# Kernel tuning notes

Hardware: AMD Instinct MI355X
Metric: run time of the kernel (lower is better)

Reference implementation:

```python
import jax, jax.numpy as jnp
import numpy as np

M, N, DIM = 128, 128, 256
BS = 8192
START_SIGMA = max(M, N) / 2.0
EPOCHS = 20.0
START_LR = 0.5
TAU = EPOCHS / np.log(START_SIGMA)


def setup_inputs() -> dict:
    key = jax.random.key(0)
    k_data, k_w = jax.random.split(key)
    data = jax.random.normal(k_data, (BS, DIM), dtype=jnp.float32)
    all_weights = jax.random.normal(k_w, (M, N, DIM), dtype=jnp.float32)
    return {"data": data, "all_weights": all_weights, "it": 3}


def reference(data, all_weights, it):
    m, n, dim = all_weights.shape
    bs = data.shape[0]

    # decayed sigma and learning rate (scalar schedule)
    sigma = START_SIGMA * jnp.exp(-jnp.float32(it) / jnp.float32(TAU))
    lr = START_LR * jnp.exp(-jnp.float32(it) / jnp.float32(EPOCHS))

    # pairwise Euclidean distances: [bs, m*n]
    w_flat = all_weights.reshape(m * n, dim)
    x_sq = jnp.sum(data * data, axis=1, keepdims=True)            # [bs, 1]
    w_sq = jnp.sum(w_flat * w_flat, axis=1)[None, :]              # [1, m*n]
    dists = jnp.sqrt(x_sq + w_sq - 2.0 * data @ w_flat.T)         # [bs, m*n]

    # best-matching unit grid coordinates (unravel over (m, n))
    bmu = jnp.argmin(dists, axis=1)                               # [bs]
    wins0 = (bmu // n).astype(jnp.float32)                        # row coord
    wins1 = (bmu % n).astype(jnp.float32)                         # col coord

    # Gaussian neighborhood around BMU, scaled by lr: [bs, m, n]
    d = 2.0 * sigma * sigma
    rows = jnp.arange(m, dtype=jnp.float32)
    cols = jnp.arange(n, dtype=jnp.float32)
    px = jnp.exp(-(rows[None, :] - wins0[:, None]) ** 2 / d)      # [bs, m]
    py = jnp.exp(-(cols[None, :] - wins1[:, None]) ** 2 / d)      # [bs, n]
    neighbor = (px[:, :, None] * py[:, None, :]) * lr             # [bs, m, n]

    # weighted batch update of the codebook
    denom = jnp.sum(neighbor, axis=0)[..., None]                  # [m, n, 1]
    numer = jnp.einsum('bk,bd->kd', neighbor.reshape(bs, m * n), data)
    numer = numer.reshape(m, n, dim)                              # [m, n, dim]
    new_weights = jnp.where(denom != 0, numer / denom, all_weights)
    return new_weights
```

## Files before the change

kernel.cpp:

```cpp
#include <hip/hip_runtime.h>
#include <hip/hip_fp16.h>

#define BS    8192
#define DIM   256
#define KTOT  16384
#define SLOTS 256
#define MARGIN 1.0f

typedef __attribute__((ext_vector_type(8))) _Float16 half8;
typedef __attribute__((ext_vector_type(4))) float f32x4;
typedef unsigned long long u64;

__device__ inline ushort f2h(float f) { return __half_as_ushort(__float2half(f)); }

__device__ inline void gload_lds16(const void* g, void* l) {
    __builtin_amdgcn_global_load_lds(
        (const __attribute__((address_space(1))) unsigned int*)g,
        (__attribute__((address_space(3))) unsigned int*)l, 16, 0, 0);
}

__device__ inline unsigned int fmap(float f) {
    unsigned int b = __float_as_uint(f);
    return (b & 0x80000000u) ? ~b : (b | 0x80000000u);
}
__device__ inline float unfmap(unsigned int m) {
    return (m & 0x80000000u) ? __uint_as_float(m & 0x7FFFFFFFu)
                             : __uint_as_float(~m);
}

__global__ void setup_all_kernel(float* __restrict__ S, float* __restrict__ G,
                                 float* __restrict__ cntf, unsigned int* __restrict__ keys,
                                 u64* __restrict__ keys2, unsigned int* __restrict__ cslot,
                                 const int* __restrict__ itp) {
    int idx = blockIdx.x * 256 + threadIdx.x;
    *(float4*)&S[(size_t)idx * 4] = make_float4(0.f, 0.f, 0.f, 0.f);
    if (idx < KTOT) {
        float itf = (float)itp[0];
        const float START_SIGMA = 64.0f;
        const float TAU = (float)(20.0 / 4.1588830833596715);
        float sigma = START_SIGMA * expf(-itf / TAU);
        float d2 = 2.0f * sigma * sigma;
        int i = idx >> 7, j = idx & 127;
        float diff = (float)(i - j);
        G[idx] = expf(-(diff * diff) / d2);
        cntf[idx] = 0.f;
    }
    if (idx < BS) { keys[idx] = 0xFFFFFFFFu; keys2[idx] = ~0ULL; cslot[idx] = 0u; }
}

__global__ void cvt_all_kernel(const float* __restrict__ x, const float* __restrict__ w,
                               ushort* __restrict__ xf, ushort* __restrict__ wf,
                               float* __restrict__ wsq) {
    int wid = threadIdx.x >> 6, lane = threadIdx.x & 63;
    int row = blockIdx.x * 4 + wid;
    int h = lane * 4;
    int window = h >> 5, c = (h >> 3) & 3, off = h & 7;
    if (row < BS) {
        int swpos = (window << 5) + (((c ^ ((row >> 1) & 3)) << 3)) + off;
        float4 v = *(const float4*)&x[(size_t)row * DIM + h];
        ushort4 hv;
        hv.x = f2h(v.x); hv.y = f2h(v.y); hv.z = f2h(v.z); hv.w = f2h(v.w);
        *(ushort4*)&xf[(size_t)row * DIM + swpos] = hv;
    } else {
        int r = row - BS;
        int swpos = (window << 5) + (((c ^ ((r >> 1) & 3)) << 3)) + off;
        float4 v = *(const float4*)&w[(size_t)r * DIM + h];
        ushort4 hv;
        hv.x = f2h(v.x); hv.y = f2h(v.y); hv.z = f2h(v.z); hv.w = f2h(v.w);
        *(ushort4*)&wf[(size_t)r * DIM + swpos] = hv;
        float s = v.x * v.x + v.y * v.y + v.z * v.z + v.w * v.w;
        #pragma unroll
        for (int o = 32; o; o >>= 1) s += __shfl_down(s, o, 64);
        if (lane == 0) wsq[r] = s;
    }
}

__global__ __launch_bounds__(256) void bmu_seed_kernel(
    const ushort* __restrict__ xf, const ushort* __restrict__ wf,
    const float* __restrict__ wsq, unsigned int* __restrict__ keys) {
    __shared__ ushort A[128 * 32];
    __shared__ ushort B[128 * 32];
    __shared__ float red[128][2];

    int m0 = blockIdx.x * 128;
    int k0 = blockIdx.y * 1024;
    int tid = threadIdx.x, w = tid >> 6, lane = tid & 63;
    int wm = (w & 1) * 64, wn = (w >> 1) * 64;
    int lm = lane & 15, quad = lane >> 4;
    int sw = (quad ^ ((lm >> 1) & 3)) * 8;
    int srow = lane >> 2, scol = (lane & 3) * 8;

    f32x4 acc[4][4];
    #pragma unroll
    for (int mi = 0; mi < 4; ++mi)
        #pragma unroll
        for (int ni = 0; ni < 4; ++ni)
            acc[mi][ni] = (f32x4){0.f, 0.f, 0.f, 0.f};

    for (int kb = 0; kb < DIM; kb += 32) {
        size_t axoff = (size_t)(m0 + w * 32 + srow) * DIM + kb + scol;
        size_t bxoff = (size_t)(k0 + w * 32 + srow) * DIM + kb + scol;
        gload_lds16(xf + axoff,            &A[(w * 32) * 32]);
        gload_lds16(xf + axoff + 16 * DIM, &A[(w * 32 + 16) * 32]);
        gload_lds16(wf + bxoff,            &B[(w * 32) * 32]);
        gload_lds16(wf + bxoff + 16 * DIM, &B[(w * 32 + 16) * 32]);
        __syncthreads();
        half8 av[4], bv[4];
        #pragma unroll
        for (int mi = 0; mi < 4; ++mi)
            av[mi] = *(const half8*)&A[(wm + mi * 16 + lm) * 32 + sw];
        #pragma unroll
        for (int ni = 0; ni < 4; ++ni)
            bv[ni] = *(const half8*)&B[(wn + ni * 16 + lm) * 32 + sw];
        #pragma unroll
        for (int mi = 0; mi < 4; ++mi)
            #pragma unroll
            for (int ni = 0; ni < 4; ++ni)
                acc[mi][ni] = __builtin_amdgcn_mfma_f32_16x16x32_f16(
                    av[mi], bv[ni], acc[mi][ni], 0, 0, 0);
        __syncthreads();
    }
    float wsqv[4];
    #pragma unroll
    for (int ni = 0; ni < 4; ++ni) wsqv[ni] = wsq[k0 + wn + ni * 16 + lm];
    #pragma unroll
    for (int mi = 0; mi < 4; ++mi)
        #pragma unroll
        for (int r = 0; r < 4; ++r) {
            float b = 3.4e38f;
            #pragma unroll
            for (int ni = 0; ni < 4; ++ni)
                b = fminf(b, fmaf(-2.0f, acc[mi][ni][r], wsqv[ni]));
            #pragma unroll
            for (int mask = 1; mask < 16; mask <<= 1)
                b = fminf(b, __shfl_xor(b, mask, 64));
            if (lm == 0) red[wm + mi * 16 + quad * 4 + r][w >> 1] = b;
        }
    __syncthreads();
    if (tid < 128)
        atomicMin(&keys[m0 + tid], fmap(fminf(red[tid][0], red[tid][1])));
}

__global__ __launch_bounds__(256) void bmu_fused_kernel(
    const ushort* __restrict__ xf, const ushort* __restrict__ wf,
    const float* __restrict__ wsq, const unsigned int* __restrict__ keys,
    unsigned int* __restrict__ cand, unsigned int* __restrict__ cslot) {
    __shared__ ushort A[128 * 32];
    __shared__ ushort B[128 * 32];
    __shared__ float thr_l[16][256];

    int m0 = blockIdx.x * 128;
    int kbase = blockIdx.y * 1024;
    int tid = threadIdx.x, w = tid >> 6, lane = tid & 63;
    int wm = (w & 1) * 64, wn = (w >> 1) * 64;
    int lm = lane & 15, quad = lane >> 4;
    int sw = (quad ^ ((lm >> 1) & 3)) * 8;
    int srow = lane >> 2, scol = (lane & 3) * 8;

    #pragma unroll
    for (int mi = 0; mi < 4; ++mi)
        #pragma unroll
        for (int r = 0; r < 4; ++r)
            thr_l[mi * 4 + r][tid] =
                unfmap(keys[m0 + wm + mi * 16 + quad * 4 + r]) + MARGIN;

    for (int kt = 0; kt < 8; ++kt) {
        int k0 = kbase + kt * 128;
        f32x4 acc[4][4];
        #pragma unroll
        for (int mi = 0; mi < 4; ++mi)
            #pragma unroll
            for (int ni = 0; ni < 4; ++ni)
                acc[mi][ni] = (f32x4){0.f, 0.f, 0.f, 0.f};

        for (int kb = 0; kb < DIM; kb += 32) {
            size_t axoff = (size_t)(m0 + w * 32 + srow) * DIM + kb + scol;
            size_t bxoff = (size_t)(k0 + w * 32 + srow) * DIM + kb + scol;
            gload_lds16(xf + axoff,            &A[(w * 32) * 32]);
            gload_lds16(xf + axoff + 16 * DIM, &A[(w * 32 + 16) * 32]);
            gload_lds16(wf + bxoff,            &B[(w * 32) * 32]);
            gload_lds16(wf + bxoff + 16 * DIM, &B[(w * 32 + 16) * 32]);
            __syncthreads();
            half8 av[4], bv[4];
            #pragma unroll
            for (int mi = 0; mi < 4; ++mi)
                av[mi] = *(const half8*)&A[(wm + mi * 16 + lm) * 32 + sw];
            #pragma unroll
            for (int ni = 0; ni < 4; ++ni)
                bv[ni] = *(const half8*)&B[(wn + ni * 16 + lm) * 32 + sw];
            #pragma unroll
            for (int mi = 0; mi < 4; ++mi)
                #pragma unroll
                for (int ni = 0; ni < 4; ++ni)
                    acc[mi][ni] = __builtin_amdgcn_mfma_f32_16x16x32_f16(
                        av[mi], bv[ni], acc[mi][ni], 0, 0, 0);
            __syncthreads();
        }
        float wsqv[4];
        #pragma unroll
        for (int ni = 0; ni < 4; ++ni) wsqv[ni] = wsq[k0 + wn + ni * 16 + lm];
        #pragma unroll
        for (int mi = 0; mi < 4; ++mi)
            #pragma unroll
            for (int r = 0; r < 4; ++r) {
                float thr = thr_l[mi * 4 + r][tid];
                #pragma unroll
                for (int ni = 0; ni < 4; ++ni) {
                    float sc = fmaf(-2.0f, acc[mi][ni][r], wsqv[ni]);
                    if (sc <= thr) {
                        unsigned int s =
                            (unsigned int)(m0 + wm + mi * 16 + quad * 4 + r);
                        unsigned int idx = atomicAdd(&cslot[s], 1u);
                        if (idx < SLOTS)
                            cand[(size_t)s * SLOTS + idx] =
                                (unsigned int)(k0 + wn + ni * 16 + lm);
                    }
                }
            }
    }
}

__global__ __launch_bounds__(256) void bmu_refine_kernel(
    const float* __restrict__ x, const float* __restrict__ w,
    const unsigned int* __restrict__ cand, const unsigned int* __restrict__ cslot,
    u64* __restrict__ keys2) {
    int lane = threadIdx.x & 63;
    int s = blockIdx.x * 4 + (threadIdx.x >> 6);
    unsigned int n = cslot[s];
    if (n > SLOTS) n = SLOTS;
    float4 xv = *(const float4*)&x[(size_t)s * DIM + lane * 4];
    u64 best = ~0ULL;
    for (unsigned int c = 0; c < n; ++c) {
        unsigned int k = cand[(size_t)s * SLOTS + c];
        float4 wv = *(const float4*)&w[(size_t)k * DIM + lane * 4];
        float dx = xv.x - wv.x, dy = xv.y - wv.y;
        float dz = xv.z - wv.z, dw = xv.w - wv.w;
        float d = dx * dx + dy * dy + dz * dz + dw * dw;
        #pragma unroll
        for (int off = 32; off; off >>= 1) d += __shfl_xor(d, off, 64);
        u64 key = ((u64)fmap(d) << 32) | (u64)k;
        best = (key < best) ? key : best;
    }
    if (lane == 0 && n > 0) keys2[s] = best;
}

__global__ __launch_bounds__(256) void scatter_kernel(
    const float* __restrict__ x, const u64* __restrict__ keys2,
    float* __restrict__ S, float* __restrict__ cntf) {
    int lane = threadIdx.x & 63;
    int s = blockIdx.x * 4 + (threadIdx.x >> 6);
    unsigned int k = (unsigned int)keys2[s];
    if (k >= KTOT) return;
    float4 xv = *(const float4*)&x[(size_t)s * DIM + lane * 4];
    float* Sp = &S[(size_t)k * DIM + lane * 4];
    atomicAdd(Sp + 0, xv.x);
    atomicAdd(Sp + 1, xv.y);
    atomicAdd(Sp + 2, xv.z);
    atomicAdd(Sp + 3, xv.w);
    if (lane == 0) atomicAdd(&cntf[k], 1.0f);
}

__global__ __launch_bounds__(256) void gemm1_kernel(
    const float* __restrict__ G, const float* __restrict__ S, float* __restrict__ T) {
    __shared__ float Sl[128 * 68];
    int n0 = blockIdx.x * 64;
    int tid = threadIdx.x;
    #pragma unroll
    for (int q = 0; q < 8; ++q) {
        int idx = q * 256 + tid;
        int row = idx >> 4, c4 = (idx & 15) * 4;
        *(float4*)&Sl[row * 68 + c4] = *(const float4*)&S[(size_t)row * 32768 + n0 + c4];
    }
    __syncthreads();
    int ng = tid & 15, ig = tid >> 4;
    for (int pass = 0; pass < 2; ++pass) {
        int ibase = pass * 64 + ig * 4;
        float acc[4][4] = {};
        for (int a = 0; a < 128; ++a) {
            float4 sv = *(const float4*)&Sl[a * 68 + ng * 4];
            #pragma unroll
            for (int ii = 0; ii < 4; ++ii) {
                float g = G[(ibase + ii) * 128 + a];
                acc[ii][0] = fmaf(g, sv.x, acc[ii][0]);
                acc[ii][1] = fmaf(g, sv.y, acc[ii][1]);
                acc[ii][2] = fmaf(g, sv.z, acc[ii][2]);
                acc[ii][3] = fmaf(g, sv.w, acc[ii][3]);
            }
        }
        #pragma unroll
        for (int ii = 0; ii < 4; ++ii)
            *(float4*)&T[(size_t)(ibase + ii) * 32768 + n0 + ng * 4] =
                *(float4*)&acc[ii][0];
    }
}

__global__ void denom_s1_kernel(const float* __restrict__ cntf, const float* __restrict__ G,
                                float* __restrict__ M1) {
    int a = blockIdx.x, j = threadIdx.x;
    float acc = 0.f;
    for (int b2 = 0; b2 < 128; ++b2)
        acc = fmaf(cntf[a * 128 + b2], G[b2 * 128 + j], acc);
    M1[a * 128 + j] = acc;
}

__global__ void denom_s2_kernel(const float* __restrict__ G, const float* __restrict__ M1,
                                float* __restrict__ denom) {
    int i = blockIdx.x, j = threadIdx.x;
    float acc = 0.f;
    for (int a = 0; a < 128; ++a)
        acc = fmaf(G[i * 128 + a], M1[a * 128 + j], acc);
    denom[i * 128 + j] = acc;
}

__global__ __launch_bounds__(256) void gemm2_fin_kernel(
    const float* __restrict__ G, const float* __restrict__ T,
    const float* __restrict__ denom, const float* __restrict__ w,
    float* __restrict__ out) {
    __shared__ float Tl[128 * 68];
    int i = blockIdx.x, dq = blockIdx.y;
    int tid = threadIdx.x;
    #pragma unroll
    for (int q = 0; q < 8; ++q) {
        int idx = q * 256 + tid;
        int row = idx >> 4, c4 = (idx & 15) * 4;
        *(float4*)&Tl[row * 68 + c4] =
            *(const float4*)&T[(size_t)i * 32768 + row * 256 + dq * 64 + c4];
    }
    __syncthreads();
    int dg = tid & 15, jg = tid >> 4;
    for (int pass = 0; pass < 2; ++pass) {
        int jbase = pass * 64 + jg * 4;
        float acc[4][4] = {};
        for (int b2 = 0; b2 < 128; ++b2) {
            float4 tv = *(const float4*)&Tl[b2 * 68 + dg * 4];
            #pragma unroll
            for (int jj = 0; jj < 4; ++jj) {
                float g = G[(jbase + jj) * 128 + b2];
                acc[jj][0] = fmaf(g, tv.x, acc[jj][0]);
                acc[jj][1] = fmaf(g, tv.y, acc[jj][1]);
                acc[jj][2] = fmaf(g, tv.z, acc[jj][2]);
                acc[jj][3] = fmaf(g, tv.w, acc[jj][3]);
            }
        }
        #pragma unroll
        for (int jj = 0; jj < 4; ++jj) {
            int j = jbase + jj;
            float dv = denom[i * 128 + j];
            size_t e = (size_t)(i * 128 + j) * DIM + dq * 64 + dg * 4;
            float4 r;
            if (dv != 0.0f) {
                float inv = 1.0f / dv;
                r.x = acc[jj][0] * inv; r.y = acc[jj][1] * inv;
                r.z = acc[jj][2] * inv; r.w = acc[jj][3] * inv;
            } else {
                r = *(const float4*)&w[e];
            }
            *(float4*)&out[e] = r;
        }
    }
}

extern "C" void kernel_launch(void* const* d_in, const int* in_sizes, int n_in,
                              void* d_out, int out_size, void* d_ws, size_t ws_size,
                              hipStream_t stream) {
    const float* data = (const float*)d_in[0];
    const float* w    = (const float*)d_in[1];
    const int*   itp  = (const int*)d_in[2];
    float* out = (float*)d_out;

    char* ws = (char*)d_ws;
    size_t off = 0;
    float*        wsq   = (float*)(ws + off);        off += 65536;
    unsigned int* keys  = (unsigned int*)(ws + off); off += 65536;
    u64*          keys2 = (u64*)(ws + off);          off += 65536;
    unsigned int* cslot = (unsigned int*)(ws + off); off += 65536;
    float*        G     = (float*)(ws + off);        off += 65536;
    float*        cntf  = (float*)(ws + off);        off += 65536;
    float*        M1    = (float*)(ws + off);        off += 65536;
    float*        denom = (float*)(ws + off);        off += 65536;
    ushort*       xf    = (ushort*)(ws + off);       off += 4194304;
    ushort*       wf    = (ushort*)(ws + off);       off += 8388608;
    u64*          spare = (u64*)(ws + off);          off += 1048576;
    float*        S     = (float*)(ws + off);        off += 16777216;
    float*        T     = (float*)(ws + off);        off += 16777216;
    unsigned int* cand  = (unsigned int*)T;
    (void)spare;

    setup_all_kernel<<<4096, 256, 0, stream>>>(S, G, cntf, keys, keys2, cslot, itp);
    cvt_all_kernel<<<(BS + KTOT) / 4, 256, 0, stream>>>(data, w, xf, wf, wsq);
    bmu_seed_kernel<<<dim3(64, 16), 256, 0, stream>>>(xf, wf, wsq, keys);
    bmu_fused_kernel<<<dim3(64, 16), 256, 0, stream>>>(xf, wf, wsq, keys, cand, cslot);
    bmu_refine_kernel<<<BS / 4, 256, 0, stream>>>(data, w, cand, cslot, keys2);
    scatter_kernel<<<BS / 4, 256, 0, stream>>>(data, keys2, S, cntf);
    gemm1_kernel<<<512, 256, 0, stream>>>(G, S, T);
    denom_s1_kernel<<<128, 128, 0, stream>>>(cntf, G, M1);
    denom_s2_kernel<<<128, 128, 0, stream>>>(G, M1, denom);
    gemm2_fin_kernel<<<dim3(128, 4), 256, 0, stream>>>(G, T, denom, w, out);
}
```

Measured before the change: 360.5 us.

## Fuse setup/convert, refine/scatter, and denominator into neighboring kernels

Merges the setup and fp16-convert kernels into one prep kernel, folds BMU refinement and scatter into a single kernel that drops the keys2 buffer, and computes the neighborhood denominator inside the final GEMM kernel instead of two separate launches. The bmu_fused threshold table shrinks from a per-thread 16x256 layout to 128 shared floats. The aim is to cut launch count and intermediate global traffic. In exchange, each of the 512 final-GEMM blocks recomputes two 128x128 mat-vec passes serially, and prep's S zeroing is now bounded by idx.

```diff
diff --git a/kernel.cpp b/kernel.cpp
--- a/kernel.cpp
+++ b/kernel.cpp
@@ -28,12 +28,15 @@
                              : __uint_as_float(~m);
 }
 
-__global__ void setup_all_kernel(float* __restrict__ S, float* __restrict__ G,
-                                 float* __restrict__ cntf, unsigned int* __restrict__ keys,
-                                 u64* __restrict__ keys2, unsigned int* __restrict__ cslot,
-                                 const int* __restrict__ itp) {
+__global__ void prep_kernel(const float* __restrict__ x, const float* __restrict__ w,
+                            ushort* __restrict__ xf, ushort* __restrict__ wf,
+                            float* __restrict__ wsq, float* __restrict__ S,
+                            float* __restrict__ G, float* __restrict__ cntf,
+                            unsigned int* __restrict__ keys, unsigned int* __restrict__ cslot,
+                            const int* __restrict__ itp) {
     int idx = blockIdx.x * 256 + threadIdx.x;
-    *(float4*)&S[(size_t)idx * 4] = make_float4(0.f, 0.f, 0.f, 0.f);
+    if (idx < 1048576)
+        *(float4*)&S[(size_t)idx * 4] = make_float4(0.f, 0.f, 0.f, 0.f);
     if (idx < KTOT) {
         float itf = (float)itp[0];
         const float START_SIGMA = 64.0f;
@@ -45,12 +48,8 @@
         G[idx] = expf(-(diff * diff) / d2);
         cntf[idx] = 0.f;
     }
-    if (idx < BS) { keys[idx] = 0xFFFFFFFFu; keys2[idx] = ~0ULL; cslot[idx] = 0u; }
-}
-
-__global__ void cvt_all_kernel(const float* __restrict__ x, const float* __restrict__ w,
-                               ushort* __restrict__ xf, ushort* __restrict__ wf,
-                               float* __restrict__ wsq) {
+    if (idx < BS) { keys[idx] = 0xFFFFFFFFu; cslot[idx] = 0u; }
+
     int wid = threadIdx.x >> 6, lane = threadIdx.x & 63;
     int row = blockIdx.x * 4 + wid;
     int h = lane * 4;
@@ -147,7 +146,7 @@
     unsigned int* __restrict__ cand, unsigned int* __restrict__ cslot) {
     __shared__ ushort A[128 * 32];
     __shared__ ushort B[128 * 32];
-    __shared__ float thr_l[16][256];
+    __shared__ float thr_l[128];
 
     int m0 = blockIdx.x * 128;
     int kbase = blockIdx.y * 1024;
@@ -157,12 +156,8 @@
     int sw = (quad ^ ((lm >> 1) & 3)) * 8;
     int srow = lane >> 2, scol = (lane & 3) * 8;
 
-    #pragma unroll
-    for (int mi = 0; mi < 4; ++mi)
-        #pragma unroll
-        for (int r = 0; r < 4; ++r)
-            thr_l[mi * 4 + r][tid] =
-                unfmap(keys[m0 + wm + mi * 16 + quad * 4 + r]) + MARGIN;
+    if (tid < 128) thr_l[tid] = unfmap(keys[m0 + tid]) + MARGIN;
+    __syncthreads();
 
     for (int kt = 0; kt < 8; ++kt) {
         int k0 = kbase + kt * 128;
@@ -203,13 +198,13 @@
         for (int mi = 0; mi < 4; ++mi)
             #pragma unroll
             for (int r = 0; r < 4; ++r) {
-                float thr = thr_l[mi * 4 + r][tid];
+                int rowi = wm + mi * 16 + quad * 4 + r;
+                float thr = thr_l[rowi];
                 #pragma unroll
                 for (int ni = 0; ni < 4; ++ni) {
                     float sc = fmaf(-2.0f, acc[mi][ni][r], wsqv[ni]);
                     if (sc <= thr) {
-                        unsigned int s =
-                            (unsigned int)(m0 + wm + mi * 16 + quad * 4 + r);
+                        unsigned int s = (unsigned int)(m0 + rowi);
                         unsigned int idx = atomicAdd(&cslot[s], 1u);
                         if (idx < SLOTS)
                             cand[(size_t)s * SLOTS + idx] =
@@ -220,10 +215,10 @@
     }
 }
 
-__global__ __launch_bounds__(256) void bmu_refine_kernel(
+__global__ __launch_bounds__(256) void refine_scatter_kernel(
     const float* __restrict__ x, const float* __restrict__ w,
     const unsigned int* __restrict__ cand, const unsigned int* __restrict__ cslot,
-    u64* __restrict__ keys2) {
+    float* __restrict__ S, float* __restrict__ cntf) {
     int lane = threadIdx.x & 63;
     int s = blockIdx.x * 4 + (threadIdx.x >> 6);
     unsigned int n = cslot[s];
@@ -241,17 +236,7 @@
         u64 key = ((u64)fmap(d) << 32) | (u64)k;
         best = (key < best) ? key : best;
     }
-    if (lane == 0 && n > 0) keys2[s] = best;
-}
-
-__global__ __launch_bounds__(256) void scatter_kernel(
-    const float* __restrict__ x, const u64* __restrict__ keys2,
-    float* __restrict__ S, float* __restrict__ cntf) {
-    int lane = threadIdx.x & 63;
-    int s = blockIdx.x * 4 + (threadIdx.x >> 6);
-    unsigned int k = (unsigned int)keys2[s];
-    if (k >= KTOT) return;
-    float4 xv = *(const float4*)&x[(size_t)s * DIM + lane * 4];
+    unsigned int k = (unsigned int)best;
     float* Sp = &S[(size_t)k * DIM + lane * 4];
     atomicAdd(Sp + 0, xv.x);
     atomicAdd(Sp + 1, xv.y);
@@ -294,37 +279,34 @@
     }
 }
 
-__global__ void denom_s1_kernel(const float* __restrict__ cntf, const float* __restrict__ G,
-                                float* __restrict__ M1) {
-    int a = blockIdx.x, j = threadIdx.x;
-    float acc = 0.f;
-    for (int b2 = 0; b2 < 128; ++b2)
-        acc = fmaf(cntf[a * 128 + b2], G[b2 * 128 + j], acc);
-    M1[a * 128 + j] = acc;
-}
-
-__global__ void denom_s2_kernel(const float* __restrict__ G, const float* __restrict__ M1,
-                                float* __restrict__ denom) {
-    int i = blockIdx.x, j = threadIdx.x;
-    float acc = 0.f;
-    for (int a = 0; a < 128; ++a)
-        acc = fmaf(G[i * 128 + a], M1[a * 128 + j], acc);
-    denom[i * 128 + j] = acc;
-}
-
 __global__ __launch_bounds__(256) void gemm2_fin_kernel(
     const float* __restrict__ G, const float* __restrict__ T,
-    const float* __restrict__ denom, const float* __restrict__ w,
+    const float* __restrict__ cntf, const float* __restrict__ w,
     float* __restrict__ out) {
     __shared__ float Tl[128 * 68];
+    __shared__ float Pl[128];
+    __shared__ float dl[128];
     int i = blockIdx.x, dq = blockIdx.y;
     int tid = threadIdx.x;
+    if (tid < 128) {
+        float p = 0.f;
+        for (int a = 0; a < 128; ++a)
+            p = fmaf(G[i * 128 + a], cntf[a * 128 + tid], p);
+        Pl[tid] = p;
+    }
     #pragma unroll
     for (int q = 0; q < 8; ++q) {
         int idx = q * 256 + tid;
         int row = idx >> 4, c4 = (idx & 15) * 4;
         *(float4*)&Tl[row * 68 + c4] =
             *(const float4*)&T[(size_t)i * 32768 + row * 256 + dq * 64 + c4];
+    }
+    __syncthreads();
+    if (tid < 128) {
+        float accd = 0.f;
+        for (int b2 = 0; b2 < 128; ++b2)
+            accd = fmaf(Pl[b2], G[b2 * 128 + tid], accd);
+        dl[tid] = accd;
     }
     __syncthreads();
     int dg = tid & 15, jg = tid >> 4;
@@ -345,7 +327,7 @@
         #pragma unroll
         for (int jj = 0; jj < 4; ++jj) {
             int j = jbase + jj;
-            float dv = denom[i * 128 + j];
+            float dv = dl[j];
             size_t e = (size_t)(i * 128 + j) * DIM + dq * 64 + dg * 4;
             float4 r;
             if (dv != 0.0f) {
@@ -372,28 +354,20 @@
     size_t off = 0;
     float*        wsq   = (float*)(ws + off);        off += 65536;
     unsigned int* keys  = (unsigned int*)(ws + off); off += 65536;
-    u64*          keys2 = (u64*)(ws + off);          off += 65536;
     unsigned int* cslot = (unsigned int*)(ws + off); off += 65536;
     float*        G     = (float*)(ws + off);        off += 65536;
     float*        cntf  = (float*)(ws + off);        off += 65536;
-    float*        M1    = (float*)(ws + off);        off += 65536;
-    float*        denom = (float*)(ws + off);        off += 65536;
     ushort*       xf    = (ushort*)(ws + off);       off += 4194304;
     ushort*       wf    = (ushort*)(ws + off);       off += 8388608;
-    u64*          spare = (u64*)(ws + off);          off += 1048576;
     float*        S     = (float*)(ws + off);        off += 16777216;
     float*        T     = (float*)(ws + off);        off += 16777216;
     unsigned int* cand  = (unsigned int*)T;
-    (void)spare;
-
-    setup_all_kernel<<<4096, 256, 0, stream>>>(S, G, cntf, keys, keys2, cslot, itp);
-    cvt_all_kernel<<<(BS + KTOT) / 4, 256, 0, stream>>>(data, w, xf, wf, wsq);
+
+    prep_kernel<<<(BS + KTOT) / 4, 256, 0, stream>>>(data, w, xf, wf, wsq,
+                                                     S, G, cntf, keys, cslot, itp);
     bmu_seed_kernel<<<dim3(64, 16), 256, 0, stream>>>(xf, wf, wsq, keys);
     bmu_fused_kernel<<<dim3(64, 16), 256, 0, stream>>>(xf, wf, wsq, keys, cand, cslot);
-    bmu_refine_kernel<<<BS / 4, 256, 0, stream>>>(data, w, cand, cslot, keys2);
-    scatter_kernel<<<BS / 4, 256, 0, stream>>>(data, keys2, S, cntf);
+    refine_scatter_kernel<<<BS / 4, 256, 0, stream>>>(data, w, cand, cslot, S, cntf);
     gemm1_kernel<<<512, 256, 0, stream>>>(G, S, T);
-    denom_s1_kernel<<<128, 128, 0, stream>>>(cntf, G, M1);
-    denom_s2_kernel<<<128, 128, 0, stream>>>(G, M1, denom);
-    gemm2_fin_kernel<<<dim3(128, 4), 256, 0, stream>>>(G, T, denom, w, out);
-}
+    gemm2_fin_kernel<<<dim3(128, 4), 256, 0, stream>>>(G, T, cntf, w, out);
+}
```

Result: faster. 330.6 us (-8.3%).
